# Kernel tuning notes

Measured on AMD Instinct MI355X. Metric: run time of the kernel, lower is better.

The kernel has to match this reference:

```python
import jax, jax.numpy as jnp
import numpy as np

N_HEAD = 16

def _proj1x1(W, b, x):
    # kernel-size-1 Conv1d == channel-wise linear: x (B, C_in, T) -> (B, C_out, T)
    return jnp.einsum('oc,bct->bot', W, x) + b[None, :, None]

def setup_inputs() -> dict:
    key = jax.random.key(0)
    B, C, T = 2, 512, 2048
    ks = jax.random.split(key, 11)
    s = 0.02
    return {
        'q': jax.random.normal(ks[0], (B, C, T), jnp.float32),
        'k': jax.random.normal(ks[1], (B, C, T), jnp.float32),
        'v': jax.random.normal(ks[2], (B, C, T), jnp.float32),
        'mask': jnp.ones((B, 1, T), dtype=bool),
        'Wq': jax.random.normal(ks[3], (C, C), jnp.float32) * s,
        'bq': jax.random.normal(ks[4], (C,), jnp.float32) * s,
        'Wk': jax.random.normal(ks[5], (C, C), jnp.float32) * s,
        'bk': jax.random.normal(ks[6], (C,), jnp.float32) * s,
        'Wv': jax.random.normal(ks[7], (C, C), jnp.float32) * s,
        'bv': jax.random.normal(ks[8], (C,), jnp.float32) * s,
        'Wp': jax.random.normal(ks[9], (C, C), jnp.float32) * s,
        'bp': jax.random.normal(ks[10], (C,), jnp.float32) * s,
    }

def reference(q, k, v, mask, Wq, bq, Wk, bk, Wv, bv, Wp, bp):
    B, C, T = q.shape
    H = N_HEAD
    D = C // H
    scale = 1.0 / np.sqrt(D).astype(np.float32)
    # 1x1 conv projections, then split heads: (B,C,T) -> (B,H,T,D)
    qh = _proj1x1(Wq, bq, q).reshape(B, H, D, T).swapaxes(2, 3)
    kh = _proj1x1(Wk, bk, k).reshape(B, H, D, T).swapaxes(2, 3)
    vh = _proj1x1(Wv, bv, v).reshape(B, H, D, T).swapaxes(2, 3)
    # scores (B,H,Tq,Tk) with key-side mask
    att = jnp.einsum('bhqd,bhkd->bhqk', qh * scale, kh)
    att = jnp.where(mask[:, :, None, :], att, -jnp.inf)
    att = jax.nn.softmax(att, axis=-1)
    # value masking (as in original: v * mask before AV matmul)
    vm = vh * mask[:, :, :, None].astype(vh.dtype)
    out = jnp.einsum('bhqk,bhkd->bhqd', att, vm)
    out = out.swapaxes(2, 3).reshape(B, C, T)
    out = _proj1x1(Wp, bp, out) * mask.astype(out.dtype)
    return (out, mask)
```

## Files before the change

### kernel.cpp

```cpp
#include <hip/hip_runtime.h>

using u16 = unsigned short;
typedef float  f32x4 __attribute__((ext_vector_type(4)));
typedef __bf16 bf8_t __attribute__((ext_vector_type(8)));
typedef u16    u16x4 __attribute__((ext_vector_type(4)));

#define NB 2
#define NH 16
#define NT 2048
#define ND 32
#define NC 512
#define QK_SCALE 0.17677669529663687f

__device__ __forceinline__ u16 f2bf(float f) {
  unsigned int u = __float_as_uint(f);
  u += 0x7fffu + ((u >> 16) & 1u);
  return (u16)(u >> 16);
}

__device__ __forceinline__ f32x4 mfma16(bf8_t a, bf8_t b, f32x4 c) {
  return __builtin_amdgcn_mfma_f32_16x16x32_bf16(a, b, c, 0, 0, 0);
}

__global__ __launch_bounds__(256) void convert_kernel(
    const float* __restrict__ Wq, const float* __restrict__ Wk,
    const float* __restrict__ Wv, const float* __restrict__ Wp,
    const void* __restrict__ mraw,
    u16* __restrict__ Wc, float* __restrict__ maskf, float* __restrict__ outtail) {
  int bid = blockIdx.x;
  if (bid < 1024) {
    int idx = (bid * 256 + (int)threadIdx.x) * 4;
    int m   = idx >> 18;
    int off = idx & 262143;
    const float* W = (m == 0) ? Wq : (m == 1) ? Wk : (m == 2) ? Wv : Wp;
    float s = (m == 0) ? QK_SCALE : 1.0f;
    f32x4 wv = *(const f32x4*)(W + off);
    u16x4 pk;
    #pragma unroll
    for (int r = 0; r < 4; ++r) pk[r] = f2bf(wv[r] * s);
    *(u16x4*)(Wc + (size_t)m * (NC * NC) + off) = pk;
  } else {
    unsigned int w0 = *(const unsigned int*)mraw;
    bool intlay = (w0 == 1u);
    #pragma unroll
    for (int kk = 0; kk < 16; ++kk) {
      int j = (int)threadIdx.x + kk * 256;
      float mv;
      if (intlay) mv = ((const int*)mraw)[j] ? 1.0f : 0.0f;
      else        mv = ((const unsigned char*)mraw)[j] ? 1.0f : 0.0f;
      maskf[j]   = mv;
      outtail[j] = mv;
    }
  }
}

__global__ __launch_bounds__(256) void transpose_kernel(
    const float* __restrict__ q, const float* __restrict__ k,
    const float* __restrict__ v, u16* __restrict__ Xt) {
  __shared__ float tile[32][33];
  int z = blockIdx.z;
  int m = z >> 1, b = z & 1;
  const float* src = (m == 0) ? q : (m == 1) ? k : v;
  int t0 = blockIdx.x * 32, c0 = blockIdx.y * 32;
  int tx = threadIdx.x, ty = threadIdx.y;
  #pragma unroll
  for (int j = 0; j < 4; ++j)
    tile[ty + j * 8][tx] = src[(size_t)(b * NC + c0 + ty + j * 8) * NT + t0 + tx];
  __syncthreads();
  u16* dst = Xt + (size_t)m * (NB * NT * NC);
  #pragma unroll
  for (int j = 0; j < 4; ++j)
    dst[((size_t)b * NT + t0 + ty + j * 8) * NC + c0 + tx] = f2bf(tile[tx][ty + j * 8]);
}

__global__ __launch_bounds__(256) void proj_kernel(
    const u16* __restrict__ Wc, const u16* __restrict__ Xt,
    const float* __restrict__ bq, const float* __restrict__ bk, const float* __restrict__ bv,
    u16* __restrict__ Qw, u16* __restrict__ Kw, u16* __restrict__ Vw,
    const float* __restrict__ maskf) {
  int z = blockIdx.z;
  const u16* W = Wc + (size_t)z * (NC * NC);
  const float* bias = (z == 0) ? bq : (z == 1) ? bk : bv;
  int tid = threadIdx.x, wid = tid >> 6, lane = tid & 63;
  int lq = lane & 15, g = lane >> 4;
  int om0 = blockIdx.x * 64;
  int b   = blockIdx.y >> 4;
  int t0  = (blockIdx.y & 15) * 128 + wid * 32;
  const u16* Xb = Xt + (size_t)z * (NB * NT * NC) + (size_t)b * NT * NC;

  const f32x4 zero = {0.f, 0.f, 0.f, 0.f};
  f32x4 acc[4][2];
  #pragma unroll
  for (int mt = 0; mt < 4; ++mt)
    #pragma unroll
    for (int nt = 0; nt < 2; ++nt) acc[mt][nt] = zero;

  for (int ks = 0; ks < 16; ++ks) {
    bf8_t af[4], bfr[2];
    #pragma unroll
    for (int mt = 0; mt < 4; ++mt)
      af[mt] = *(const bf8_t*)(W + (size_t)(om0 + mt * 16 + lq) * NC + ks * 32 + 8 * g);
    #pragma unroll
    for (int nt = 0; nt < 2; ++nt)
      bfr[nt] = *(const bf8_t*)(Xb + (size_t)(t0 + nt * 16 + lq) * NC + ks * 32 + 8 * g);
    #pragma unroll
    for (int mt = 0; mt < 4; ++mt)
      #pragma unroll
      for (int nt = 0; nt < 2; ++nt)
        acc[mt][nt] = mfma16(af[mt], bfr[nt], acc[mt][nt]);
  }

  float sc = (z == 0) ? QK_SCALE : 1.0f;
  #pragma unroll
  for (int mt = 0; mt < 4; ++mt) {
    int ob = om0 + mt * 16 + 4 * g;
    float b4[4];
    #pragma unroll
    for (int r = 0; r < 4; ++r) b4[r] = bias[ob + r] * sc;
    #pragma unroll
    for (int nt = 0; nt < 2; ++nt) {
      int t = t0 + nt * 16 + lq;
      if (z < 2) {
        u16x4 pk;
        #pragma unroll
        for (int r = 0; r < 4; ++r) pk[r] = f2bf(acc[mt][nt][r] + b4[r]);
        u16* dst = (z == 0) ? Qw : Kw;
        *(u16x4*)(dst + ((size_t)(b * NH + (ob >> 5)) * NT + t) * ND + (ob & 31)) = pk;
      } else {
        float mv = maskf[b * NT + t];
        #pragma unroll
        for (int r = 0; r < 4; ++r)
          Vw[(size_t)(b * NC + ob + r) * NT + t] = f2bf((acc[mt][nt][r] + b4[r]) * mv);
      }
    }
  }
}

__global__ __launch_bounds__(256) void attn_kernel(
    const u16* __restrict__ Qw, const u16* __restrict__ Kw, const u16* __restrict__ Vw,
    u16* __restrict__ Ow, const float* __restrict__ maskf) {
  __shared__ u16 plds[4][32][128];
  int tid = threadIdx.x, wid = tid >> 6, lane = tid & 63;
  int lq = lane & 15, g = lane >> 4;
  int bh = blockIdx.y, b = bh >> 4, h = bh & 15;
  int q0 = blockIdx.x * 128 + wid * 32;
  const u16* Qb = Qw + (size_t)bh * NT * ND;
  const u16* Kb = Kw + (size_t)bh * NT * ND;
  const u16* Vb = Vw + (size_t)(b * NC + h * ND) * NT;
  const float* mfp = maskf + b * NT;
  char* pbase = (char*)&plds[wid][0][0];

  bf8_t qf[2];
  #pragma unroll
  for (int c = 0; c < 2; ++c)
    qf[c] = *(const bf8_t*)(Qb + (size_t)(q0 + c * 16 + lq) * ND + 8 * g);

  const f32x4 zero = {0.f, 0.f, 0.f, 0.f};
  f32x4 acc[2][2];
  #pragma unroll
  for (int dt = 0; dt < 2; ++dt)
    #pragma unroll
    for (int c = 0; c < 2; ++c) acc[dt][c] = zero;
  float mrun[2] = {-1e30f, -1e30f}, lrun[2] = {0.f, 0.f};

  for (int kt = 0; kt < 16; ++kt) {
    int tkb = kt * 128;
    f32x4 st[8][2];
    #pragma unroll
    for (int rt = 0; rt < 8; ++rt) {
      bf8_t kf = *(const bf8_t*)(Kb + (size_t)(tkb + rt * 16 + lq) * ND + 8 * g);
      st[rt][0] = mfma16(kf, qf[0], zero);
      st[rt][1] = mfma16(kf, qf[1], zero);
    }
    #pragma unroll
    for (int rt = 0; rt < 8; ++rt) {
      f32x4 mb = *(const f32x4*)(mfp + tkb + rt * 16 + 4 * g);
      #pragma unroll
      for (int r = 0; r < 4; ++r) {
        float mbias = (mb[r] - 1.0f) * 1e30f;
        st[rt][0][r] += mbias;
        st[rt][1][r] += mbias;
      }
    }
    #pragma unroll
    for (int c = 0; c < 2; ++c) {
      float tm = -1e30f;
      #pragma unroll
      for (int rt = 0; rt < 8; ++rt)
        #pragma unroll
        for (int r = 0; r < 4; ++r) tm = fmaxf(tm, st[rt][c][r]);
      tm = fmaxf(tm, __shfl_xor(tm, 16));
      tm = fmaxf(tm, __shfl_xor(tm, 32));
      float mnew = fmaxf(mrun[c], tm);
      float al = __expf(mrun[c] - mnew);
      mrun[c] = mnew;
      float rs = 0.f;
      #pragma unroll
      for (int rt = 0; rt < 8; ++rt)
        #pragma unroll
        for (int r = 0; r < 4; ++r) {
          float p = __expf(st[rt][c][r] - mnew);
          st[rt][c][r] = p;
          rs += p;
        }
      rs += __shfl_xor(rs, 16);
      rs += __shfl_xor(rs, 32);
      lrun[c] = lrun[c] * al + rs;
      acc[0][c] *= al;
      acc[1][c] *= al;
    }
    #pragma unroll
    for (int rt = 0; rt < 8; ++rt)
      #pragma unroll
      for (int c = 0; c < 2; ++c) {
        int row = c * 16 + lq;
        u16x4 pk;
        #pragma unroll
        for (int r = 0; r < 4; ++r) pk[r] = f2bf(st[rt][c][r]);
        *(u16x4*)(pbase + row * 256 + ((rt * 32 + 8 * g) ^ ((row & 7) << 4))) = pk;
      }
    #pragma unroll
    for (int kk = 0; kk < 4; ++kk) {
      bf8_t pf[2];
      #pragma unroll
      for (int c = 0; c < 2; ++c) {
        int row = c * 16 + lq;
        pf[c] = *(const bf8_t*)(pbase + row * 256 + ((kk * 64 + 16 * g) ^ ((row & 7) << 4)));
      }
      #pragma unroll
      for (int dt = 0; dt < 2; ++dt) {
        bf8_t vf = *(const bf8_t*)(Vb + (size_t)(dt * 16 + lq) * NT + tkb + kk * 32 + 8 * g);
        acc[dt][0] = mfma16(vf, pf[0], acc[dt][0]);
        acc[dt][1] = mfma16(vf, pf[1], acc[dt][1]);
      }
    }
  }
  #pragma unroll
  for (int c = 0; c < 2; ++c) {
    float inv = 1.0f / lrun[c];
    int t = q0 + c * 16 + lq;
    #pragma unroll
    for (int dt = 0; dt < 2; ++dt) {
      u16x4 o;
      #pragma unroll
      for (int r = 0; r < 4; ++r) o[r] = f2bf(acc[dt][c][r] * inv);
      *(u16x4*)(Ow + ((size_t)bh * NT + t) * ND + dt * 16 + 4 * g) = o;
    }
  }
}

__global__ __launch_bounds__(256) void outproj_kernel(
    const u16* __restrict__ Wc, const u16* __restrict__ Ow,
    const float* __restrict__ bp, float* __restrict__ out,
    const float* __restrict__ maskf) {
  const u16* W = Wc + (size_t)3 * NC * NC;
  int tid = threadIdx.x, wid = tid >> 6, lane = tid & 63;
  int lq = lane & 15, g = lane >> 4;
  int om0 = blockIdx.x * 64;
  int b   = blockIdx.y >> 4;
  int t0  = (blockIdx.y & 15) * 128 + wid * 32;
  const u16* Ob = Ow + (size_t)b * NH * NT * ND;

  const f32x4 zero = {0.f, 0.f, 0.f, 0.f};
  f32x4 acc[4][2];
  #pragma unroll
  for (int mt = 0; mt < 4; ++mt)
    #pragma unroll
    for (int nt = 0; nt < 2; ++nt) acc[mt][nt] = zero;

  for (int ks = 0; ks < 16; ++ks) {
    bf8_t af[4], bfr[2];
    #pragma unroll
    for (int mt = 0; mt < 4; ++mt)
      af[mt] = *(const bf8_t*)(W + (size_t)(om0 + mt * 16 + lq) * NC + ks * 32 + 8 * g);
    #pragma unroll
    for (int nt = 0; nt < 2; ++nt)
      bfr[nt] = *(const bf8_t*)(Ob + ((size_t)ks * NT + t0 + nt * 16 + lq) * ND + 8 * g);
    #pragma unroll
    for (int mt = 0; mt < 4; ++mt)
      #pragma unroll
      for (int nt = 0; nt < 2; ++nt)
        acc[mt][nt] = mfma16(af[mt], bfr[nt], acc[mt][nt]);
  }
  #pragma unroll
  for (int mt = 0; mt < 4; ++mt) {
    int ob = om0 + mt * 16 + 4 * g;
    float b4[4];
    #pragma unroll
    for (int r = 0; r < 4; ++r) b4[r] = bp[ob + r];
    #pragma unroll
    for (int nt = 0; nt < 2; ++nt) {
      int t = t0 + nt * 16 + lq;
      float mv = maskf[b * NT + t];
      #pragma unroll
      for (int r = 0; r < 4; ++r)
        out[(size_t)(b * NC + ob + r) * NT + t] = (acc[mt][nt][r] + b4[r]) * mv;
    }
  }
}

extern "C" void kernel_launch(void* const* d_in, const int* in_sizes, int n_in,
                              void* d_out, int out_size, void* d_ws, size_t ws_size,
                              hipStream_t stream) {
  const float* q  = (const float*)d_in[0];
  const float* k  = (const float*)d_in[1];
  const float* v  = (const float*)d_in[2];
  const void*  mr = d_in[3];
  const float* Wq = (const float*)d_in[4];
  const float* bq = (const float*)d_in[5];
  const float* Wk = (const float*)d_in[6];
  const float* bk = (const float*)d_in[7];
  const float* Wv = (const float*)d_in[8];
  const float* bv = (const float*)d_in[9];
  const float* Wp = (const float*)d_in[10];
  const float* bp = (const float*)d_in[11];
  float* out = (float*)d_out;

  u16* Wc = (u16*)d_ws;
  u16* Xt = Wc + (size_t)4 * NC * NC;
  u16* Qw = Xt + (size_t)3 * NB * NT * NC;
  u16* Kw = Qw + (size_t)NB * NT * NC;
  u16* Vw = Kw + (size_t)NB * NT * NC;
  u16* Ow = Vw + (size_t)NB * NT * NC;
  float* maskf   = (float*)(Ow + (size_t)NB * NT * NC);
  float* outtail = out + (size_t)NB * NC * NT;

  convert_kernel<<<1025, 256, 0, stream>>>(Wq, Wk, Wv, Wp, mr, Wc, maskf, outtail);
  transpose_kernel<<<dim3(NT / 32, NC / 32, 6), dim3(32, 8), 0, stream>>>(q, k, v, Xt);
  proj_kernel<<<dim3(8, 32, 3), 256, 0, stream>>>(Wc, Xt, bq, bk, bv, Qw, Kw, Vw, maskf);
  attn_kernel<<<dim3(16, 32), 256, 0, stream>>>(Qw, Kw, Vw, Ow, maskf);
  outproj_kernel<<<dim3(8, 32), 256, 0, stream>>>(Wc, Ow, bp, out, maskf);
}
```

Before: 208.2 us.

## Streamline attention softmax with exp2, lazy rescale, MFMA row sums and mask bias

Folds log2(e) into the Q scale so the softmax can use exp2 directly, and precomputes an additive mask bias that is fed into the QK MFMA as its accumulator. Row-max rescaling now runs only when some lane's max grows by more than a threshold, and the row sum comes from an extra MFMA against a ones vector instead of shuffles. V fragments are loaded early so their latency overlaps the softmax, and bf16 packing uses the hardware pack-convert instruction. The cost is extra MFMA work and registers, plus some precision risk from the threshold-based rescaling.

```diff
diff --git a/kernel.cpp b/kernel.cpp
--- a/kernel.cpp
+++ b/kernel.cpp
@@ -4,6 +4,7 @@
 typedef float  f32x4 __attribute__((ext_vector_type(4)));
 typedef __bf16 bf8_t __attribute__((ext_vector_type(8)));
 typedef u16    u16x4 __attribute__((ext_vector_type(4)));
+typedef unsigned int u32x2 __attribute__((ext_vector_type(2)));
 
 #define NB 2
 #define NH 16
@@ -11,6 +12,7 @@
 #define ND 32
 #define NC 512
 #define QK_SCALE 0.17677669529663687f
+#define LOG2E    1.4426950408889634f
 
 __device__ __forceinline__ u16 f2bf(float f) {
   unsigned int u = __float_as_uint(f);
@@ -18,6 +20,12 @@
   return (u16)(u >> 16);
 }
 
+__device__ __forceinline__ unsigned int cvt_pk_bf16(float a, float b) {
+  unsigned int r;
+  asm("v_cvt_pk_bf16_f32 %0, %1, %2" : "=v"(r) : "v"(a), "v"(b));
+  return r;
+}
+
 __device__ __forceinline__ f32x4 mfma16(bf8_t a, bf8_t b, f32x4 c) {
   return __builtin_amdgcn_mfma_f32_16x16x32_bf16(a, b, c, 0, 0, 0);
 }
@@ -26,14 +34,15 @@
     const float* __restrict__ Wq, const float* __restrict__ Wk,
     const float* __restrict__ Wv, const float* __restrict__ Wp,
     const void* __restrict__ mraw,
-    u16* __restrict__ Wc, float* __restrict__ maskf, float* __restrict__ outtail) {
+    u16* __restrict__ Wc, float* __restrict__ maskf, float* __restrict__ maskb,
+    float* __restrict__ outtail) {
   int bid = blockIdx.x;
   if (bid < 1024) {
     int idx = (bid * 256 + (int)threadIdx.x) * 4;
     int m   = idx >> 18;
     int off = idx & 262143;
     const float* W = (m == 0) ? Wq : (m == 1) ? Wk : (m == 2) ? Wv : Wp;
-    float s = (m == 0) ? QK_SCALE : 1.0f;
+    float s = (m == 0) ? (QK_SCALE * LOG2E) : 1.0f;
     f32x4 wv = *(const f32x4*)(W + off);
     u16x4 pk;
     #pragma unroll
@@ -49,6 +58,7 @@
       if (intlay) mv = ((const int*)mraw)[j] ? 1.0f : 0.0f;
       else        mv = ((const unsigned char*)mraw)[j] ? 1.0f : 0.0f;
       maskf[j]   = mv;
+      maskb[j]   = (mv - 1.0f) * 1e30f;
       outtail[j] = mv;
     }
   }
@@ -110,7 +120,7 @@
         acc[mt][nt] = mfma16(af[mt], bfr[nt], acc[mt][nt]);
   }
 
-  float sc = (z == 0) ? QK_SCALE : 1.0f;
+  float sc = (z == 0) ? (QK_SCALE * LOG2E) : 1.0f;
   #pragma unroll
   for (int mt = 0; mt < 4; ++mt) {
     int ob = om0 + mt * 16 + 4 * g;
@@ -138,7 +148,7 @@
 
 __global__ __launch_bounds__(256) void attn_kernel(
     const u16* __restrict__ Qw, const u16* __restrict__ Kw, const u16* __restrict__ Vw,
-    u16* __restrict__ Ow, const float* __restrict__ maskf) {
+    u16* __restrict__ Ow, const float* __restrict__ maskb) {
   __shared__ u16 plds[4][32][128];
   int tid = threadIdx.x, wid = tid >> 6, lane = tid & 63;
   int lq = lane & 15, g = lane >> 4;
@@ -147,8 +157,12 @@
   const u16* Qb = Qw + (size_t)bh * NT * ND;
   const u16* Kb = Kw + (size_t)bh * NT * ND;
   const u16* Vb = Vw + (size_t)(b * NC + h * ND) * NT;
-  const float* mfp = maskf + b * NT;
+  const float* mbp = maskb + b * NT;
   char* pbase = (char*)&plds[wid][0][0];
+
+  bf8_t ones;
+  #pragma unroll
+  for (int j = 0; j < 8; ++j) ones[j] = (__bf16)1.0f;
 
   bf8_t qf[2];
   #pragma unroll
@@ -156,69 +170,60 @@
     qf[c] = *(const bf8_t*)(Qb + (size_t)(q0 + c * 16 + lq) * ND + 8 * g);
 
   const f32x4 zero = {0.f, 0.f, 0.f, 0.f};
-  f32x4 acc[2][2];
-  #pragma unroll
-  for (int dt = 0; dt < 2; ++dt)
+  f32x4 acc[3][2];
+  #pragma unroll
+  for (int dt = 0; dt < 3; ++dt)
     #pragma unroll
     for (int c = 0; c < 2; ++c) acc[dt][c] = zero;
-  float mrun[2] = {-1e30f, -1e30f}, lrun[2] = {0.f, 0.f};
+  float mrun[2] = {0.f, 0.f};
 
   for (int kt = 0; kt < 16; ++kt) {
     int tkb = kt * 128;
     f32x4 st[8][2];
     #pragma unroll
     for (int rt = 0; rt < 8; ++rt) {
+      f32x4 bias = *(const f32x4*)(mbp + tkb + rt * 16 + 4 * g);
       bf8_t kf = *(const bf8_t*)(Kb + (size_t)(tkb + rt * 16 + lq) * ND + 8 * g);
-      st[rt][0] = mfma16(kf, qf[0], zero);
-      st[rt][1] = mfma16(kf, qf[1], zero);
-    }
-    #pragma unroll
-    for (int rt = 0; rt < 8; ++rt) {
-      f32x4 mb = *(const f32x4*)(mfp + tkb + rt * 16 + 4 * g);
-      #pragma unroll
-      for (int r = 0; r < 4; ++r) {
-        float mbias = (mb[r] - 1.0f) * 1e30f;
-        st[rt][0][r] += mbias;
-        st[rt][1][r] += mbias;
-      }
-    }
+      st[rt][0] = mfma16(kf, qf[0], bias);
+      st[rt][1] = mfma16(kf, qf[1], bias);
+    }
+    bf8_t vf[2][4];
+    #pragma unroll
+    for (int dt = 0; dt < 2; ++dt)
+      #pragma unroll
+      for (int kk = 0; kk < 4; ++kk)
+        vf[dt][kk] = *(const bf8_t*)(Vb + (size_t)(dt * 16 + lq) * NT + tkb + kk * 32 + 8 * g);
+
     #pragma unroll
     for (int c = 0; c < 2; ++c) {
       float tm = -1e30f;
       #pragma unroll
-      for (int rt = 0; rt < 8; ++rt)
-        #pragma unroll
-        for (int r = 0; r < 4; ++r) tm = fmaxf(tm, st[rt][c][r]);
+      for (int rt = 0; rt < 8; ++rt) {
+        tm = fmaxf(fmaxf(st[rt][c][0], st[rt][c][1]), tm);
+        tm = fmaxf(fmaxf(st[rt][c][2], st[rt][c][3]), tm);
+      }
       tm = fmaxf(tm, __shfl_xor(tm, 16));
       tm = fmaxf(tm, __shfl_xor(tm, 32));
-      float mnew = fmaxf(mrun[c], tm);
-      float al = __expf(mrun[c] - mnew);
-      mrun[c] = mnew;
-      float rs = 0.f;
-      #pragma unroll
-      for (int rt = 0; rt < 8; ++rt)
-        #pragma unroll
-        for (int r = 0; r < 4; ++r) {
-          float p = __expf(st[rt][c][r] - mnew);
-          st[rt][c][r] = p;
-          rs += p;
-        }
-      rs += __shfl_xor(rs, 16);
-      rs += __shfl_xor(rs, 32);
-      lrun[c] = lrun[c] * al + rs;
-      acc[0][c] *= al;
-      acc[1][c] *= al;
-    }
-    #pragma unroll
-    for (int rt = 0; rt < 8; ++rt)
-      #pragma unroll
-      for (int c = 0; c < 2; ++c) {
-        int row = c * 16 + lq;
-        u16x4 pk;
-        #pragma unroll
-        for (int r = 0; r < 4; ++r) pk[r] = f2bf(st[rt][c][r]);
-        *(u16x4*)(pbase + row * 256 + ((rt * 32 + 8 * g) ^ ((row & 7) << 4))) = pk;
-      }
+      if (__any(tm > mrun[c] + 8.0f)) {
+        float mnew = fmaxf(mrun[c], tm);
+        float al = __builtin_amdgcn_exp2f(mrun[c] - mnew);
+        mrun[c] = mnew;
+        acc[0][c] *= al; acc[1][c] *= al; acc[2][c] *= al;
+      }
+      float nm = -mrun[c];
+      int row = c * 16 + lq;
+      #pragma unroll
+      for (int rt = 0; rt < 8; ++rt) {
+        float p0 = __builtin_amdgcn_exp2f(st[rt][c][0] + nm);
+        float p1 = __builtin_amdgcn_exp2f(st[rt][c][1] + nm);
+        float p2 = __builtin_amdgcn_exp2f(st[rt][c][2] + nm);
+        float p3 = __builtin_amdgcn_exp2f(st[rt][c][3] + nm);
+        u32x2 w;
+        w[0] = cvt_pk_bf16(p0, p1);
+        w[1] = cvt_pk_bf16(p2, p3);
+        *(u32x2*)(pbase + row * 256 + ((rt * 32 + 8 * g) ^ ((row & 7) << 4))) = w;
+      }
+    }
     #pragma unroll
     for (int kk = 0; kk < 4; ++kk) {
       bf8_t pf[2];
@@ -228,23 +233,23 @@
         pf[c] = *(const bf8_t*)(pbase + row * 256 + ((kk * 64 + 16 * g) ^ ((row & 7) << 4)));
       }
       #pragma unroll
-      for (int dt = 0; dt < 2; ++dt) {
-        bf8_t vf = *(const bf8_t*)(Vb + (size_t)(dt * 16 + lq) * NT + tkb + kk * 32 + 8 * g);
-        acc[dt][0] = mfma16(vf, pf[0], acc[dt][0]);
-        acc[dt][1] = mfma16(vf, pf[1], acc[dt][1]);
+      for (int c = 0; c < 2; ++c) {
+        acc[0][c] = mfma16(vf[0][kk], pf[c], acc[0][c]);
+        acc[1][c] = mfma16(vf[1][kk], pf[c], acc[1][c]);
+        acc[2][c] = mfma16(ones,      pf[c], acc[2][c]);
       }
     }
   }
   #pragma unroll
   for (int c = 0; c < 2; ++c) {
-    float inv = 1.0f / lrun[c];
+    float inv = 1.0f / acc[2][c][0];
     int t = q0 + c * 16 + lq;
     #pragma unroll
     for (int dt = 0; dt < 2; ++dt) {
-      u16x4 o;
-      #pragma unroll
-      for (int r = 0; r < 4; ++r) o[r] = f2bf(acc[dt][c][r] * inv);
-      *(u16x4*)(Ow + ((size_t)bh * NT + t) * ND + dt * 16 + 4 * g) = o;
+      u32x2 o;
+      o[0] = cvt_pk_bf16(acc[dt][c][0] * inv, acc[dt][c][1] * inv);
+      o[1] = cvt_pk_bf16(acc[dt][c][2] * inv, acc[dt][c][3] * inv);
+      *(u32x2*)(Ow + ((size_t)bh * NT + t) * ND + dt * 16 + 4 * g) = o;
     }
   }
 }
@@ -323,11 +328,12 @@
   u16* Vw = Kw + (size_t)NB * NT * NC;
   u16* Ow = Vw + (size_t)NB * NT * NC;
   float* maskf   = (float*)(Ow + (size_t)NB * NT * NC);
+  float* maskb   = maskf + (size_t)NB * NT;
   float* outtail = out + (size_t)NB * NC * NT;
 
-  convert_kernel<<<1025, 256, 0, stream>>>(Wq, Wk, Wv, Wp, mr, Wc, maskf, outtail);
+  convert_kernel<<<1025, 256, 0, stream>>>(Wq, Wk, Wv, Wp, mr, Wc, maskf, maskb, outtail);
   transpose_kernel<<<dim3(NT / 32, NC / 32, 6), dim3(32, 8), 0, stream>>>(q, k, v, Xt);
   proj_kernel<<<dim3(8, 32, 3), 256, 0, stream>>>(Wc, Xt, bq, bk, bv, Qw, Kw, Vw, maskf);
-  attn_kernel<<<dim3(16, 32), 256, 0, stream>>>(Qw, Kw, Vw, Ow, maskf);
+  attn_kernel<<<dim3(16, 32), 256, 0, stream>>>(Qw, Kw, Vw, Ow, maskb);
   outproj_kernel<<<dim3(8, 32), 256, 0, stream>>>(Wc, Ow, bp, out, maskf);
 }
```

Result: faster. 203.9 us (-2.1%).
